# Kernel tuning notes

Measured on AMD Instinct MI355X. Metric: run time of the kernel, lower is better.

The kernel has to match this reference:

```python
import jax, jax.numpy as jnp
import numpy as np

N_NODES = 50000
N_EDGES = 400000
C = 32            # channels per irrep (scalars and l=1 vectors)
N_BASIS = 8
HID = 64          # radial MLP hidden dim
N_LAYERS = 2
N_SPECIES = 86
N_GRAPHS = 64
R_MAX = 5.0
EPS = 1e-5


def setup_inputs() -> dict:
    key = jax.random.key(0)
    ks = jax.random.split(key, 16)
    species = jax.random.randint(ks[0], (N_NODES,), 0, N_SPECIES)
    pos = jax.random.normal(ks[1], (N_NODES, 3), jnp.float32)
    edge_index = jax.random.randint(ks[2], (2, N_EDGES), 0, N_NODES)
    batch = jnp.sort(jax.random.randint(ks[3], (N_NODES,), 0, N_GRAPHS))

    emb = jax.random.normal(ks[4], (N_SPECIES, C), jnp.float32) * 0.1
    freqs = jnp.arange(1, N_BASIS + 1, dtype=jnp.float32) * jnp.pi / R_MAX  # trainable Bessel freqs
    rW1 = jax.random.normal(ks[5], (N_LAYERS, N_BASIS, HID), jnp.float32) / np.sqrt(N_BASIS)
    rb1 = jnp.zeros((N_LAYERS, HID), jnp.float32)
    rW2 = jax.random.normal(ks[6], (N_LAYERS, HID, HID), jnp.float32) / np.sqrt(HID)
    rb2 = jnp.zeros((N_LAYERS, HID), jnp.float32)
    rW3 = jax.random.normal(ks[7], (N_LAYERS, HID, 4 * C), jnp.float32) / np.sqrt(HID)
    rb3 = jnp.zeros((N_LAYERS, 4 * C), jnp.float32)
    Wss = jax.random.normal(ks[8], (N_LAYERS, C, C), jnp.float32) / np.sqrt(C)
    bss = jnp.zeros((N_LAYERS, C), jnp.float32)
    Wvv = jax.random.normal(ks[9], (N_LAYERS, C, C), jnp.float32) / np.sqrt(C)
    bn_gs = jnp.ones((N_LAYERS, C), jnp.float32)
    bn_bs = jnp.zeros((N_LAYERS, C), jnp.float32)
    bn_gv = jnp.ones((N_LAYERS, C), jnp.float32)
    W_out = jax.random.normal(ks[10], (C, 1), jnp.float32) / np.sqrt(C)
    b_out = jnp.zeros((1,), jnp.float32)
    atom_ref = jnp.zeros((N_SPECIES, 1), jnp.float32)  # AtomRef init zeros
    return dict(species=species, pos=pos, edge_index=edge_index, batch=batch,
                emb=emb, freqs=freqs, rW1=rW1, rb1=rb1, rW2=rW2, rb2=rb2,
                rW3=rW3, rb3=rb3, Wss=Wss, bss=bss, Wvv=Wvv,
                bn_gs=bn_gs, bn_bs=bn_bs, bn_gv=bn_gv,
                W_out=W_out, b_out=b_out, atom_ref=atom_ref)


def _bessel_basis(dist, freqs):
    # basis = sin(f*r)/r with smooth polynomial cutoff (as in BesselRadialBasis.forward)
    d = jnp.clip(dist, 0.0)
    basis = jnp.sin(freqs[None, :] * d[:, None]) / jnp.clip(d, 1e-6)[:, None]
    x = jnp.clip(d / R_MAX, 0.0, 1.0)
    cut = 1.0 - 6.0 * x ** 5 + 15.0 * x ** 4 - 10.0 * x ** 3
    cut = jnp.where(d <= R_MAX, cut, 0.0)
    return basis * cut[:, None]


def _forward(species, pos, edge_index, batch, emb, freqs, rW1, rb1, rW2, rb2,
             rW3, rb3, Wss, bss, Wvv, bn_gs, bn_bs, bn_gv, W_out, b_out, atom_ref):
    src, dst = edge_index[0], edge_index[1]
    vec = pos[dst] - pos[src]                      # (E,3) edge vectors
    dist = jnp.sqrt(jnp.sum(vec * vec, axis=-1))   # (E,)
    basis = _bessel_basis(dist, freqs)             # (E,NB)
    Y1 = vec / jnp.clip(dist, 1e-9)[:, None]       # (E,3) l=1 spherical harmonics (unit dir)

    s = emb[species]                               # (N,C) scalar features
    v = jnp.zeros((s.shape[0], C, 3), s.dtype)     # (N,C,3) l=1 features

    for l in range(N_LAYERS):
        # radial MLP -> per-edge channel-wise tensor-product weights (4 paths x C)
        h = jax.nn.silu(basis @ rW1[l] + rb1[l])
        h = jax.nn.silu(h @ rW2[l] + rb2[l])
        w = h @ rW3[l] + rb3[l]                    # (E,4C)
        w1, w2, w3, w4 = jnp.split(w, 4, axis=-1)  # each (E,C)

        xs = s[src]                                # (E,C)   gather
        xv = v[src]                                # (E,C,3) gather
        # TP paths: s*Y0 -> scalar; (v.Y1) -> gate scalar; s*Y1 -> vector; v*Y0 -> vector
        m_sf = w1 * xs                                               # (E,C)
        m_sg = w2 * jnp.einsum('ecd,ed->ec', xv, Y1)                 # (E,C)
        m_v = w3[..., None] * xs[..., None] * Y1[:, None, :] + w4[..., None] * xv  # (E,C,3)

        agg_sf = jax.ops.segment_sum(m_sf, dst, num_segments=N_NODES)
        agg_sg = jax.ops.segment_sum(m_sg, dst, num_segments=N_NODES)
        agg_v = jax.ops.segment_sum(m_v, dst, num_segments=N_NODES)

        # gated nonlinearity: silu on scalars, sigmoid gate on vectors
        s_new = jax.nn.silu(agg_sf)
        v_new = jax.nn.sigmoid(agg_sg)[..., None] * agg_v

        # self-interaction (equivariant linear mixing over channels)
        s_new = s_new @ Wss[l] + bss[l]
        v_new = jnp.einsum('ncd,cm->nmd', v_new, Wvv[l])

        # e3nn-style batch norm: standardize scalars; norm-normalize vectors
        mu = jnp.mean(s_new, axis=0)
        var = jnp.mean((s_new - mu) ** 2, axis=0)
        s_new = (s_new - mu) / jnp.sqrt(var + EPS) * bn_gs[l] + bn_bs[l]
        vnorm2 = jnp.mean(jnp.sum(v_new * v_new, axis=-1), axis=0) / 3.0  # per-channel, /(2l+1)
        v_new = v_new / jnp.sqrt(vnorm2 + EPS)[None, :, None] * bn_gv[l][None, :, None]

        # residual (irreps match)
        s = s + s_new
        v = v + v_new

    node_e = s @ W_out + b_out                                       # (N,1)
    graph_e = jax.ops.segment_sum(node_e, batch, num_segments=N_GRAPHS)
    ref_e = jax.ops.segment_sum(atom_ref[species], batch, num_segments=N_GRAPHS)
    return graph_e + ref_e                                           # (B,1)


def reference(species, pos, edge_index, batch, emb, freqs, rW1, rb1, rW2, rb2,
              rW3, rb3, Wss, bss, Wvv, bn_gs, bn_bs, bn_gv, W_out, b_out, atom_ref):
    return _forward(species, pos, edge_index, batch, emb, freqs, rW1, rb1, rW2, rb2,
                    rW3, rb3, Wss, bss, Wvv, bn_gs, bn_bs, bn_gv, W_out, b_out, atom_ref)
```

## Files before the change

### kernel.cpp

```cpp
#include <hip/hip_runtime.h>
#include <math.h>

#define N_NODES 50000
#define N_EDGES 400000
#define C 32
#define NB 8
#define HID 64
#define NL 2
#define NG 64
#define RMAXF 5.0f
#define EPSF 1e-5f
#define TBL 4096
#define BN_BLOCKS 512
#define NBLK_N ((N_NODES + 255) / 256)

__device__ __forceinline__ float silu_f(float x) { return x / (1.0f + __expf(-x)); }
__device__ __forceinline__ float sigmoid_f(float x) { return 1.0f / (1.0f + __expf(-x)); }
__device__ __forceinline__ void atomAddF(float* p, float val) {
  __hip_atomic_fetch_add(p, val, __ATOMIC_RELAXED, __HIP_MEMORY_SCOPE_AGENT);
}
__device__ __forceinline__ void atomAddD(double* p, double val) {
  __hip_atomic_fetch_add(p, val, __ATOMIC_RELAXED, __HIP_MEMORY_SCOPE_AGENT);
}
__device__ __forceinline__ unsigned short bf16_rne(float f) {
  unsigned u = __float_as_uint(f);
  return (unsigned short)((u + 0x7FFFu + ((u >> 16) & 1u)) >> 16);
}
__device__ __forceinline__ float bfu(unsigned short u) {
  return __uint_as_float(((unsigned)u) << 16);
}

__global__ __launch_bounds__(256) void k_edge_geom(
    const float* __restrict__ pos, const int* __restrict__ ei,
    const float* __restrict__ freqs,
    float* __restrict__ basis, float* __restrict__ Y1)
{
  int e = blockIdx.x * 256 + threadIdx.x;
  if (e >= N_EDGES) return;
  int s = ei[e], d = ei[N_EDGES + e];
  float vx = pos[d*3+0] - pos[s*3+0];
  float vy = pos[d*3+1] - pos[s*3+1];
  float vz = pos[d*3+2] - pos[s*3+2];
  float dist = sqrtf(vx*vx + vy*vy + vz*vz);
  float invd = 1.0f / fmaxf(dist, 1e-9f);
  Y1[e*3+0] = vx*invd; Y1[e*3+1] = vy*invd; Y1[e*3+2] = vz*invd;
  float x = fminf(fmaxf(dist * (1.0f/RMAXF), 0.0f), 1.0f);
  float x2 = x*x, x3 = x2*x;
  float cut = 1.0f - x3 * (10.0f - 15.0f*x + 6.0f*x2);
  if (dist > RMAXF) cut = 0.0f;
  float rinv = cut / fmaxf(dist, 1e-6f);
  #pragma unroll
  for (int k = 0; k < NB; k++)
    basis[e*NB + k] = sinf(freqs[k] * dist) * rinv;
}

__global__ __launch_bounds__(256) void k_node_init(
    const int* __restrict__ species, const float* __restrict__ emb,
    float* __restrict__ s, unsigned short* __restrict__ s_bf)
{
  int i = blockIdx.x * 256 + threadIdx.x;
  if (i >= N_NODES * C) return;
  int n = i >> 5, c = i & 31;
  float x = emb[species[n]*C + c];
  s[i] = x;
  s_bf[i] = bf16_rne(x);
}

__global__ __launch_bounds__(256) void k_hist(const int* __restrict__ ei, int* __restrict__ counts)
{
  int e = blockIdx.x * 256 + threadIdx.x;
  if (e >= N_EDGES) return;
  atomicAdd(&counts[ei[N_EDGES + e]], 1);
}

__global__ __launch_bounds__(256) void k_scanA(const int* __restrict__ counts, int* __restrict__ bsum)
{
  __shared__ int sh[256];
  int i = blockIdx.x * 256 + threadIdx.x;
  int x = (i < N_NODES) ? counts[i] : 0;
  sh[threadIdx.x] = x;
  __syncthreads();
  for (int off = 128; off > 0; off >>= 1) {
    if (threadIdx.x < off) sh[threadIdx.x] += sh[threadIdx.x + off];
    __syncthreads();
  }
  if (threadIdx.x == 0) bsum[blockIdx.x] = sh[0];
}

__global__ __launch_bounds__(256) void k_scanB(int* __restrict__ bsum)
{
  __shared__ int sh[256];
  int tid = threadIdx.x;
  int x = (tid < NBLK_N) ? bsum[tid] : 0;
  sh[tid] = x;
  __syncthreads();
  for (int off = 1; off < 256; off <<= 1) {
    int y = (tid >= off) ? sh[tid - off] : 0;
    __syncthreads();
    sh[tid] += y;
    __syncthreads();
  }
  if (tid < NBLK_N) bsum[tid] = sh[tid] - x;
}

__global__ __launch_bounds__(256) void k_scanC(const int* __restrict__ counts,
                                               const int* __restrict__ bsum,
                                               int* __restrict__ row_start)
{
  __shared__ int sh[256];
  int i = blockIdx.x * 256 + threadIdx.x;
  int x = (i < N_NODES) ? counts[i] : 0;
  sh[threadIdx.x] = x;
  __syncthreads();
  for (int off = 1; off < 256; off <<= 1) {
    int y = (threadIdx.x >= off) ? sh[threadIdx.x - off] : 0;
    __syncthreads();
    sh[threadIdx.x] += y;
    __syncthreads();
  }
  if (i < N_NODES) row_start[i] = bsum[blockIdx.x] + sh[threadIdx.x] - x;
}

__global__ __launch_bounds__(256) void k_geom_scatter(
    const float* __restrict__ pos, const int* __restrict__ ei,
    const int* __restrict__ row_start, int* __restrict__ cursor,
    float* __restrict__ rec)
{
  int e = blockIdx.x * 256 + threadIdx.x;
  if (e >= N_EDGES) return;
  int s = ei[e], d = ei[N_EDGES + e];
  float vx = pos[d*3+0] - pos[s*3+0];
  float vy = pos[d*3+1] - pos[s*3+1];
  float vz = pos[d*3+2] - pos[s*3+2];
  float dist = sqrtf(vx*vx + vy*vy + vz*vz);
  float invd = 1.0f / fmaxf(dist, 1e-9f);
  int p = row_start[d] + atomicAdd(&cursor[d], 1);
  float* rp = rec + (size_t)p * 8;
  float4 r0; r0.x = dist; r0.y = __int_as_float(s); r0.z = vx*invd; r0.w = vy*invd;
  *(float4*)rp = r0;
  rp[4] = vz*invd;
}

__global__ __launch_bounds__(256) void k_table_h(
    const float* __restrict__ freqs,
    const float* __restrict__ rW1, const float* __restrict__ rb1,
    const float* __restrict__ rW2, const float* __restrict__ rb2,
    float* __restrict__ h2tab)
{
  int idx = blockIdx.x * 256 + threadIdx.x;
  if (idx >= NL * TBL) return;
  int l = idx / TBL, i = idx - l * TBL;
  float d = (float)i * (RMAXF / (float)(TBL - 1));
  float x = fminf(fmaxf(d * (1.0f/RMAXF), 0.0f), 1.0f);
  float x2 = x*x, x3 = x2*x;
  float cut = 1.0f - x3 * (10.0f - 15.0f*x + 6.0f*x2);
  float rinv = cut / fmaxf(d, 1e-6f);
  float bas[NB];
  #pragma unroll
  for (int k = 0; k < NB; k++) bas[k] = sinf(freqs[k] * d) * rinv;

  const float* W1 = rW1 + l*NB*HID;
  const float* B1 = rb1 + l*HID;
  const float* W2 = rW2 + l*HID*HID;
  const float* B2 = rb2 + l*HID;

  float h2[HID];
  #pragma unroll
  for (int j = 0; j < HID; j++) h2[j] = B2[j];
  #pragma unroll 2
  for (int k = 0; k < HID; k++) {
    float t = B1[k];
    #pragma unroll
    for (int b = 0; b < NB; b++) t = fmaf(bas[b], W1[b*HID + k], t);
    float h1k = silu_f(t);
    const float* r = W2 + k*HID;
    #pragma unroll
    for (int j = 0; j < HID; j++) h2[j] = fmaf(h1k, r[j], h2[j]);
  }
  float* out = h2tab + (size_t)idx * HID;
  #pragma unroll
  for (int j = 0; j < HID; j++) out[j] = silu_f(h2[j]);
}

__global__ __launch_bounds__(256) void k_table_w(
    const float* __restrict__ h2tab,
    const float* __restrict__ rW3, const float* __restrict__ rb3,
    float* __restrict__ wtab)
{
  int idx = blockIdx.x * 256 + threadIdx.x;
  if (idx >= NL * TBL * 16) return;
  int chunk = idx & 15;
  int row   = idx >> 4;
  int l     = row / TBL;
  const float* h2 = h2tab + (size_t)row * HID;
  const float* W3 = rW3 + l*HID*4*C + chunk*8;
  const float* B3 = rb3 + l*4*C + chunk*8;
  float a[8];
  #pragma unroll
  for (int ci = 0; ci < 8; ci++) a[ci] = B3[ci];
  #pragma unroll 4
  for (int k = 0; k < HID; k++) {
    float h = h2[k];
    #pragma unroll
    for (int ci = 0; ci < 8; ci++) a[ci] = fmaf(h, W3[k*4*C + ci], a[ci]);
  }
  float* out = wtab + (size_t)row * 128 + chunk*8;
  #pragma unroll
  for (int ci = 0; ci < 8; ci++) out[ci] = a[ci];
}

__global__ __launch_bounds__(256) void k_agg_update(
    const float* __restrict__ tb,
    const float* __restrict__ rec,
    const int* __restrict__ row_start, const int* __restrict__ counts,
    const unsigned short* __restrict__ s_bf, const unsigned short* __restrict__ v_bf,
    const float* __restrict__ Wss, const float* __restrict__ bss,
    const float* __restrict__ Wvv,
    float* __restrict__ s_new, float* __restrict__ v_new)
{
  int t = blockIdx.x * 256 + threadIdx.x;
  int n = t >> 5;
  int c = t & 31;

  const float SCALE = (float)(TBL - 1) / RMAXF;
  float asf = 0.0f, asg = 0.0f, av0 = 0.0f, av1 = 0.0f, av2 = 0.0f;
  int beg = row_start[n], cnt = counts[n];

  if (cnt > 0) {
    int last = beg + cnt - 1;
    int pA = beg, pB = (beg + 1 < last) ? beg + 1 : last;
    float4 rA = *(const float4*)(rec + (size_t)pA * 8);
    float  zA = rec[(size_t)pA * 8 + 4];
    float4 rB = *(const float4*)(rec + (size_t)pB * 8);
    float  zB = rec[(size_t)pB * 8 + 4];

    for (int i = 0; i < cnt; i += 2) {
      int pA2 = beg + i + 2; pA2 = pA2 < last ? pA2 : last;
      int pB2 = beg + i + 3; pB2 = pB2 < last ? pB2 : last;
      float4 rA_n = *(const float4*)(rec + (size_t)pA2 * 8);
      float  zA_n = rec[(size_t)pA2 * 8 + 4];
      float4 rB_n = *(const float4*)(rec + (size_t)pB2 * 8);
      float  zB_n = rec[(size_t)pB2 * 8 + 4];

      float validB = (i + 1 < cnt) ? 1.0f : 0.0f;
      float dA = rA.x;  int srcA = __float_as_int(rA.y);
      float yA0 = rA.z, yA1 = rA.w, yA2 = zA;
      float dB = rB.x;  int srcB = __float_as_int(rB.y);
      float yB0 = rB.z, yB1 = rB.w, yB2 = zB;

      float xsA = bfu(s_bf[srcA*C + c]);
      const unsigned short* vpA = v_bf + (size_t)(srcA*C + c)*3;
      float xvA0 = bfu(vpA[0]), xvA1 = bfu(vpA[1]), xvA2 = bfu(vpA[2]);
      float xsB = bfu(s_bf[srcB*C + c]);
      const unsigned short* vpB = v_bf + (size_t)(srcB*C + c)*3;
      float xvB0 = bfu(vpB[0]), xvB1 = bfu(vpB[1]), xvB2 = bfu(vpB[2]);

      float tsA = fminf(dA, RMAXF) * SCALE;
      int t0A = (int)tsA; t0A = t0A > TBL-2 ? TBL-2 : t0A;
      float frA = tsA - (float)t0A;
      float tsB = fminf(dB, RMAXF) * SCALE;
      int t0B = (int)tsB; t0B = t0B > TBL-2 ? TBL-2 : t0B;
      float frB = tsB - (float)t0B;

      const float* rtA0 = tb + (size_t)t0A * 128 + c;
      const float* rtA1 = rtA0 + 128;
      const float* rtB0 = tb + (size_t)t0B * 128 + c;
      const float* rtB1 = rtB0 + 128;

      float w1A = fmaf(frA, rtA1[0]  - rtA0[0],  rtA0[0]);
      float w2A = fmaf(frA, rtA1[32] - rtA0[32], rtA0[32]);
      float w3A = fmaf(frA, rtA1[64] - rtA0[64], rtA0[64]);
      float w4A = fmaf(frA, rtA1[96] - rtA0[96], rtA0[96]);
      float w1B = validB * fmaf(frB, rtB1[0]  - rtB0[0],  rtB0[0]);
      float w2B = validB * fmaf(frB, rtB1[32] - rtB0[32], rtB0[32]);
      float w3B = validB * fmaf(frB, rtB1[64] - rtB0[64], rtB0[64]);
      float w4B = validB * fmaf(frB, rtB1[96] - rtB0[96], rtB0[96]);

      asf = fmaf(w1A, xsA, asf);
      asg = fmaf(w2A, xvA0*yA0 + xvA1*yA1 + xvA2*yA2, asg);
      float w3xsA = w3A * xsA;
      av0 += fmaf(w3xsA, yA0, w4A*xvA0);
      av1 += fmaf(w3xsA, yA1, w4A*xvA1);
      av2 += fmaf(w3xsA, yA2, w4A*xvA2);

      asf = fmaf(w1B, xsB, asf);
      asg = fmaf(w2B, xvB0*yB0 + xvB1*yB1 + xvB2*yB2, asg);
      float w3xsB = w3B * xsB;
      av0 += fmaf(w3xsB, yB0, w4B*xvB0);
      av1 += fmaf(w3xsB, yB1, w4B*xvB1);
      av2 += fmaf(w3xsB, yB2, w4B*xvB2);

      rA = rA_n; zA = zA_n; rB = rB_n; zB = zB_n;
    }
  }

  float sgv  = silu_f(asf);
  float gate = sigmoid_f(asg);
  float vg0 = gate*av0, vg1 = gate*av1, vg2 = gate*av2;

  float sn = bss[c];
  float vm0 = 0.0f, vm1 = 0.0f, vm2 = 0.0f;
  #pragma unroll
  for (int k = 0; k < C; k++) {
    float a  = __shfl(sgv, k, 32);
    sn = fmaf(a, Wss[k*C + c], sn);
    float wv = Wvv[k*C + c];
    vm0 = fmaf(__shfl(vg0, k, 32), wv, vm0);
    vm1 = fmaf(__shfl(vg1, k, 32), wv, vm1);
    vm2 = fmaf(__shfl(vg2, k, 32), wv, vm2);
  }

  s_new[n*C + c] = sn;
  float* vo = v_new + (size_t)(n*C + c)*3;
  vo[0] = vm0; vo[1] = vm1; vo[2] = vm2;
}

__global__ __launch_bounds__(256) void k_bn_stats(
    const float* __restrict__ s_new, const float* __restrict__ v_new,
    double* __restrict__ bn_sums)
{
  __shared__ float lacc[3*C];
  if (threadIdx.x < 3*C) lacc[threadIdx.x] = 0.0f;
  __syncthreads();
  int c = threadIdx.x & 31;
  float r1 = 0.0f, r2 = 0.0f, r3 = 0.0f;
  const int NC = N_NODES * C;
  for (int i = blockIdx.x * 256 + threadIdx.x; i < NC; i += BN_BLOCKS * 256) {
    float sn = s_new[i];
    const float* vp = v_new + (size_t)i * 3;
    r1 += sn;
    r2 += sn * sn;
    r3 += vp[0]*vp[0] + vp[1]*vp[1] + vp[2]*vp[2];
  }
  atomicAdd(&lacc[c],       r1);
  atomicAdd(&lacc[C + c],   r2);
  atomicAdd(&lacc[2*C + c], r3);
  __syncthreads();
  if (threadIdx.x < 3*C) atomAddD(&bn_sums[threadIdx.x], (double)lacc[threadIdx.x]);
}

__global__ __launch_bounds__(256) void k_apply(
    const float* __restrict__ s_new, const float* __restrict__ v_new,
    const double* __restrict__ bn_sums,
    const float* __restrict__ gs, const float* __restrict__ gv,
    const float* __restrict__ bn_bs,
    float* __restrict__ s, float* __restrict__ v,
    unsigned short* __restrict__ s_bf, unsigned short* __restrict__ v_bf)
{
  int i = blockIdx.x * 256 + threadIdx.x;
  if (i >= N_NODES * C) return;
  int c = i & 31;
  double S1 = bn_sums[c], S2 = bn_sums[C + c], VN = bn_sums[2*C + c];
  float mu  = (float)(S1 / (double)N_NODES);
  float var = (float)(S2 / (double)N_NODES) - mu*mu;
  float vn2 = (float)(VN / (3.0 * (double)N_NODES));
  float ssc = gs[c] / sqrtf(var + EPSF);
  float vsc = gv[c] / sqrtf(vn2 + EPSF);

  float sv = s[i] + (s_new[i] - mu) * ssc + bn_bs[c];
  s[i] = sv;
  s_bf[i] = bf16_rne(sv);
  float* vp = v + (size_t)i*3;
  const float* vn = v_new + (size_t)i*3;
  unsigned short* vb = v_bf + (size_t)i*3;
  #pragma unroll
  for (int d = 0; d < 3; d++) {
    float vv = vp[d] + vn[d] * vsc;
    vp[d] = vv;
    vb[d] = bf16_rne(vv);
  }
}

__global__ __launch_bounds__(256) void k_readout(
    const float* __restrict__ s, const int* __restrict__ species,
    const int* __restrict__ batch,
    const float* __restrict__ W_out, const float* __restrict__ b_out,
    const float* __restrict__ atom_ref, float* __restrict__ out)
{
  __shared__ float acc[NG];
  if (threadIdx.x < NG) acc[threadIdx.x] = 0.0f;
  __syncthreads();
  int n = blockIdx.x * 256 + threadIdx.x;
  if (n < N_NODES) {
    float e = b_out[0] + atom_ref[species[n]];
    #pragma unroll
    for (int c = 0; c < C; c++) e = fmaf(s[n*C + c], W_out[c], e);
    atomicAdd(&acc[batch[n]], e);
  }
  __syncthreads();
  if (threadIdx.x < NG) {
    float a = acc[threadIdx.x];
    if (a != 0.0f) atomAddF(&out[threadIdx.x], a);
  }
}

__global__ __launch_bounds__(256) void k_edge_msg_fb(
    const float* __restrict__ basis, const float* __restrict__ Y1,
    const int* __restrict__ ei,
    const float* __restrict__ s, const float* __restrict__ v,
    const float* __restrict__ rW1, const float* __restrict__ rb1,
    const float* __restrict__ rW2, const float* __restrict__ rb2,
    const float* __restrict__ rW3, const float* __restrict__ rb3,
    float* __restrict__ agg_sf, float* __restrict__ agg_sg, float* __restrict__ agg_v)
{
  int e = blockIdx.x * 256 + threadIdx.x;
  if (e >= N_EDGES) return;
  int src = ei[e], dst = ei[N_EDGES + e];
  const float4 b0 = *(const float4*)(basis + (size_t)e*NB);
  const float4 b1 = *(const float4*)(basis + (size_t)e*NB + 4);
  float bas[NB] = {b0.x, b0.y, b0.z, b0.w, b1.x, b1.y, b1.z, b1.w};
  float h2[HID];
  #pragma unroll
  for (int j = 0; j < HID; j++) h2[j] = rb2[j];
  #pragma unroll 2
  for (int k = 0; k < HID; k++) {
    float t = rb1[k];
    #pragma unroll
    for (int b = 0; b < NB; b++) t = fmaf(bas[b], rW1[b*HID + k], t);
    float h1k = silu_f(t);
    const float* r = rW2 + k*HID;
    #pragma unroll
    for (int j = 0; j < HID; j++) h2[j] = fmaf(h1k, r[j], h2[j]);
  }
  #pragma unroll
  for (int j = 0; j < HID; j++) h2[j] = silu_f(h2[j]);
  float y0 = Y1[e*3+0], y1 = Y1[e*3+1], y2 = Y1[e*3+2];
  #pragma unroll 1
  for (int cb = 0; cb < 16; cb++) {
    float a[8];
    #pragma unroll
    for (int ci = 0; ci < 8; ci++) a[ci] = rb3[cb*8 + ci];
    #pragma unroll
    for (int k = 0; k < HID; k++) {
      float h = h2[k];
      #pragma unroll
      for (int ci = 0; ci < 8; ci++) a[ci] = fmaf(h, rW3[k*4*C + cb*8 + ci], a[ci]);
    }
    #pragma unroll
    for (int ci = 0; ci < 8; ci++) {
      int o = cb*8 + ci;
      int path = o >> 5;
      int c = o & 31;
      float xs = s[src*C + c];
      const float* vp = v + (size_t)(src*C + c)*3;
      float xv0 = vp[0], xv1 = vp[1], xv2 = vp[2];
      if (path == 0) {
        atomAddF(&agg_sf[dst*C + c], a[ci] * xs);
      } else if (path == 1) {
        atomAddF(&agg_sg[dst*C + c], a[ci] * (xv0*y0 + xv1*y1 + xv2*y2));
      } else if (path == 2) {
        float w3xs = a[ci] * xs;
        float* ap = agg_v + (size_t)(dst*C + c)*3;
        atomAddF(ap+0, w3xs*y0); atomAddF(ap+1, w3xs*y1); atomAddF(ap+2, w3xs*y2);
      } else {
        float* ap = agg_v + (size_t)(dst*C + c)*3;
        atomAddF(ap+0, a[ci]*xv0); atomAddF(ap+1, a[ci]*xv1); atomAddF(ap+2, a[ci]*xv2);
      }
    }
  }
}

__global__ __launch_bounds__(256) void k_node_update_fb(
    const float* __restrict__ agg_sf, const float* __restrict__ agg_sg,
    const float* __restrict__ agg_v,
    const float* __restrict__ Wss, const float* __restrict__ bss,
    const float* __restrict__ Wvv,
    float* __restrict__ s_new, float* __restrict__ v_new,
    double* __restrict__ bn_sums)
{
  __shared__ float lacc[3*C];
  int t = blockIdx.x * 256 + threadIdx.x;
  int n = t >> 5;
  int c = t & 31;
  if (threadIdx.x < 3*C) lacc[threadIdx.x] = 0.0f;
  __syncthreads();
  float asf = agg_sf[n*C + c];
  float asg = agg_sg[n*C + c];
  const float* ap = agg_v + (size_t)(n*C + c)*3;
  float av0 = ap[0], av1 = ap[1], av2 = ap[2];
  float sgv = silu_f(asf);
  float gate = sigmoid_f(asg);
  float vg0 = gate*av0, vg1 = gate*av1, vg2 = gate*av2;
  float sn = bss[c];
  float vm0 = 0.0f, vm1 = 0.0f, vm2 = 0.0f;
  #pragma unroll
  for (int k = 0; k < C; k++) {
    float a  = __shfl(sgv, k, 32);
    sn = fmaf(a, Wss[k*C + c], sn);
    float wv = Wvv[k*C + c];
    vm0 = fmaf(__shfl(vg0, k, 32), wv, vm0);
    vm1 = fmaf(__shfl(vg1, k, 32), wv, vm1);
    vm2 = fmaf(__shfl(vg2, k, 32), wv, vm2);
  }
  s_new[n*C + c] = sn;
  float* vo = v_new + (size_t)(n*C + c)*3;
  vo[0] = vm0; vo[1] = vm1; vo[2] = vm2;
  float vn2 = vm0*vm0 + vm1*vm1 + vm2*vm2;
  atomicAdd(&lacc[c], sn);
  atomicAdd(&lacc[C + c], sn*sn);
  atomicAdd(&lacc[2*C + c], vn2);
  __syncthreads();
  if (threadIdx.x < 3*C) atomAddD(&bn_sums[threadIdx.x], (double)lacc[threadIdx.x]);
}

__global__ void k_bn_scales_fb(const double* __restrict__ bn_sums,
                               const float* __restrict__ gs, const float* __restrict__ gv,
                               float* __restrict__ scales)
{
  int m = threadIdx.x;
  if (m >= C) return;
  double S1 = bn_sums[m], S2 = bn_sums[C + m], VN = bn_sums[2*C + m];
  double mu  = S1 / (double)N_NODES;
  double var = S2 / (double)N_NODES - mu*mu;
  double vn2 = VN / (3.0 * (double)N_NODES);
  scales[m]       = (float)mu;
  scales[C + m]   = gs[m] / sqrtf((float)var + EPSF);
  scales[2*C + m] = gv[m] / sqrtf((float)vn2 + EPSF);
}

__global__ __launch_bounds__(256) void k_apply_fb(
    const float* __restrict__ s_new, const float* __restrict__ v_new,
    const float* __restrict__ scales, const float* __restrict__ bn_bs,
    float* __restrict__ s, float* __restrict__ v)
{
  int i = blockIdx.x * 256 + threadIdx.x;
  if (i >= N_NODES * C) return;
  int c = i & 31;
  s[i] += (s_new[i] - scales[c]) * scales[C + c] + bn_bs[c];
  float vs = scales[2*C + c];
  v[(size_t)i*3+0] += v_new[(size_t)i*3+0] * vs;
  v[(size_t)i*3+1] += v_new[(size_t)i*3+1] * vs;
  v[(size_t)i*3+2] += v_new[(size_t)i*3+2] * vs;
}

extern "C" void kernel_launch(void* const* d_in, const int* in_sizes, int n_in,
                              void* d_out, int out_size, void* d_ws, size_t ws_size,
                              hipStream_t stream)
{
  const int*   species  = (const int*)  d_in[0];
  const float* pos      = (const float*)d_in[1];
  const int*   ei       = (const int*)  d_in[2];
  const int*   batch    = (const int*)  d_in[3];
  const float* emb      = (const float*)d_in[4];
  const float* freqs    = (const float*)d_in[5];
  const float* rW1      = (const float*)d_in[6];
  const float* rb1      = (const float*)d_in[7];
  const float* rW2      = (const float*)d_in[8];
  const float* rb2      = (const float*)d_in[9];
  const float* rW3      = (const float*)d_in[10];
  const float* rb3      = (const float*)d_in[11];
  const float* Wss      = (const float*)d_in[12];
  const float* bss      = (const float*)d_in[13];
  const float* Wvv      = (const float*)d_in[14];
  const float* bn_gs    = (const float*)d_in[15];
  const float* bn_bs    = (const float*)d_in[16];
  const float* bn_gv    = (const float*)d_in[17];
  const float* W_out    = (const float*)d_in[18];
  const float* b_out    = (const float*)d_in[19];
  const float* atom_ref = (const float*)d_in[20];

  float* ws = (float*)d_ws;
  size_t off = 0;
  float* basis  = ws + off; off += (size_t)N_EDGES * NB;
  float* Y1     = ws + off; off += (size_t)N_EDGES * 3;
  float* s      = ws + off; off += (size_t)N_NODES * C;
  float* v      = ws + off; off += (size_t)N_NODES * C * 3;
  float* s_new  = ws + off; off += (size_t)N_NODES * C;
  float* v_new  = ws + off; off += (size_t)N_NODES * C * 3;
  double* bn_sums = (double*)(ws + off); off += 192;
  float* scales = ws + off; off += 96;

  size_t ra = off;
  float* rec      = ws + ra;            ra += (size_t)N_EDGES * 8;
  int*   counts   = (int*)(ws + ra);    ra += N_NODES;
  int*   row_start= (int*)(ws + ra);    ra += N_NODES;
  int*   cursor   = (int*)(ws + ra);    ra += N_NODES;
  int*   bsum     = (int*)(ws + ra);    ra += 256;
  float* h2tab    = ws + ra;            ra += (size_t)NL * TBL * HID;
  float* wtab     = ws + ra;            ra += (size_t)NL * TBL * 128;
  unsigned short* s_bf = (unsigned short*)(ws + ra); ra += (size_t)N_NODES * C / 2;
  unsigned short* v_bf = (unsigned short*)(ws + ra); ra += (size_t)N_NODES * C * 3 / 2;
  size_t req_sorted = ra * 4;

  size_t rb = off;
  float* agg_sf = ws + rb; rb += (size_t)N_NODES * C;
  float* agg_sg = ws + rb; rb += (size_t)N_NODES * C;
  float* agg_v  = ws + rb; rb += (size_t)N_NODES * C * 3;

  dim3 b256(256);
  const int gE  = (N_EDGES + 255) / 256;
  const int gNC = (N_NODES * C + 255) / 256;
  const int gN  = (N_NODES + 255) / 256;

  hipMemsetAsync(v, 0, (size_t)N_NODES * C * 3 * sizeof(float), stream);

  if (ws_size >= req_sorted) {
    hipMemsetAsync(v_bf, 0, (size_t)N_NODES * C * 3 * sizeof(unsigned short), stream);
    hipMemsetAsync(counts, 0, N_NODES * sizeof(int), stream);
    hipMemsetAsync(cursor, 0, N_NODES * sizeof(int), stream);
    k_node_init<<<gNC, b256, 0, stream>>>(species, emb, s, s_bf);
    k_hist<<<gE, b256, 0, stream>>>(ei, counts);
    k_scanA<<<NBLK_N, b256, 0, stream>>>(counts, bsum);
    k_scanB<<<1, b256, 0, stream>>>(bsum);
    k_scanC<<<NBLK_N, b256, 0, stream>>>(counts, bsum, row_start);
    k_geom_scatter<<<gE, b256, 0, stream>>>(pos, ei, row_start, cursor, rec);
    k_table_h<<<(NL*TBL)/256, b256, 0, stream>>>(freqs, rW1, rb1, rW2, rb2, h2tab);
    k_table_w<<<(NL*TBL*16)/256, b256, 0, stream>>>(h2tab, rW3, rb3, wtab);

    for (int l = 0; l < NL; l++) {
      hipMemsetAsync(bn_sums, 0, 96 * sizeof(double), stream);
      k_agg_update<<<(N_NODES*C)/256, b256, 0, stream>>>(
          wtab + (size_t)l * TBL * 128, rec,
          row_start, counts, s_bf, v_bf, Wss + l*C*C, bss + l*C, Wvv + l*C*C,
          s_new, v_new);
      k_bn_stats<<<BN_BLOCKS, b256, 0, stream>>>(s_new, v_new, bn_sums);
      k_apply<<<gNC, b256, 0, stream>>>(s_new, v_new, bn_sums,
          bn_gs + l*C, bn_gv + l*C, bn_bs + l*C, s, v, s_bf, v_bf);
    }
  } else {
    k_node_init<<<gNC, b256, 0, stream>>>(species, emb, s, (unsigned short*)(ws + off));
    k_edge_geom<<<gE, b256, 0, stream>>>(pos, ei, freqs, basis, Y1);
    for (int l = 0; l < NL; l++) {
      hipMemsetAsync(agg_sf, 0, (size_t)N_NODES * 5 * C * sizeof(float), stream);
      hipMemsetAsync(bn_sums, 0, 96 * sizeof(double), stream);
      k_edge_msg_fb<<<gE, b256, 0, stream>>>(basis, Y1, ei, s, v,
          rW1 + l*NB*HID, rb1 + l*HID, rW2 + l*HID*HID, rb2 + l*HID,
          rW3 + l*HID*4*C, rb3 + l*4*C, agg_sf, agg_sg, agg_v);
      k_node_update_fb<<<(N_NODES*C)/256, b256, 0, stream>>>(agg_sf, agg_sg, agg_v,
          Wss + l*C*C, bss + l*C, Wvv + l*C*C, s_new, v_new, bn_sums);
      k_bn_scales_fb<<<1, 64, 0, stream>>>(bn_sums, bn_gs + l*C, bn_gv + l*C, scales);
      k_apply_fb<<<gNC, b256, 0, stream>>>(s_new, v_new, scales, bn_bs + l*C, s, v);
    }
  }

  hipMemsetAsync(d_out, 0, NG * sizeof(float), stream);
  k_readout<<<gN, b256, 0, stream>>>(s, species, batch, W_out, b_out, atom_ref, (float*)d_out);
}
```

Before: 321.2 us.

## Specialize first layer for zero vectors, pad bf16 vectors, fuse readout into apply

The aggregation kernel is templated on whether vector features exist. Layer 0 therefore skips the vector gathers and the w2/w4 table loads, since v starts at zero. Vector bf16 storage is padded to 4 halves so each gather is a single ushort4 load, and the first apply writes v directly instead of needing a memset. The readout is fused into the last apply kernel through a wave shuffle reduction plus one atomic per node, which removes a separate kernel and several memsets at the cost of more atomics and 33% more vector bf16 memory.

```diff
diff --git a/kernel.cpp b/kernel.cpp
--- a/kernel.cpp
+++ b/kernel.cpp
@@ -209,11 +209,12 @@
   for (int ci = 0; ci < 8; ci++) out[ci] = a[ci];
 }
 
+template<bool HAS_V>
 __global__ __launch_bounds__(256) void k_agg_update(
     const float* __restrict__ tb,
     const float* __restrict__ rec,
     const int* __restrict__ row_start, const int* __restrict__ counts,
-    const unsigned short* __restrict__ s_bf, const unsigned short* __restrict__ v_bf,
+    const unsigned short* __restrict__ s_bf, const unsigned short* __restrict__ v_bf4,
     const float* __restrict__ Wss, const float* __restrict__ bss,
     const float* __restrict__ Wvv,
     float* __restrict__ s_new, float* __restrict__ v_new)
@@ -249,11 +250,15 @@
       float yB0 = rB.z, yB1 = rB.w, yB2 = zB;
 
       float xsA = bfu(s_bf[srcA*C + c]);
-      const unsigned short* vpA = v_bf + (size_t)(srcA*C + c)*3;
-      float xvA0 = bfu(vpA[0]), xvA1 = bfu(vpA[1]), xvA2 = bfu(vpA[2]);
       float xsB = bfu(s_bf[srcB*C + c]);
-      const unsigned short* vpB = v_bf + (size_t)(srcB*C + c)*3;
-      float xvB0 = bfu(vpB[0]), xvB1 = bfu(vpB[1]), xvB2 = bfu(vpB[2]);
+      float xvA0 = 0.0f, xvA1 = 0.0f, xvA2 = 0.0f;
+      float xvB0 = 0.0f, xvB1 = 0.0f, xvB2 = 0.0f;
+      if (HAS_V) {
+        ushort4 a4 = *(const ushort4*)(v_bf4 + (size_t)(srcA*C + c)*4);
+        ushort4 b4 = *(const ushort4*)(v_bf4 + (size_t)(srcB*C + c)*4);
+        xvA0 = bfu(a4.x); xvA1 = bfu(a4.y); xvA2 = bfu(a4.z);
+        xvB0 = bfu(b4.x); xvB1 = bfu(b4.y); xvB2 = bfu(b4.z);
+      }
 
       float tsA = fminf(dA, RMAXF) * SCALE;
       int t0A = (int)tsA; t0A = t0A > TBL-2 ? TBL-2 : t0A;
@@ -268,27 +273,30 @@
       const float* rtB1 = rtB0 + 128;
 
       float w1A = fmaf(frA, rtA1[0]  - rtA0[0],  rtA0[0]);
-      float w2A = fmaf(frA, rtA1[32] - rtA0[32], rtA0[32]);
       float w3A = fmaf(frA, rtA1[64] - rtA0[64], rtA0[64]);
-      float w4A = fmaf(frA, rtA1[96] - rtA0[96], rtA0[96]);
       float w1B = validB * fmaf(frB, rtB1[0]  - rtB0[0],  rtB0[0]);
-      float w2B = validB * fmaf(frB, rtB1[32] - rtB0[32], rtB0[32]);
       float w3B = validB * fmaf(frB, rtB1[64] - rtB0[64], rtB0[64]);
-      float w4B = validB * fmaf(frB, rtB1[96] - rtB0[96], rtB0[96]);
 
       asf = fmaf(w1A, xsA, asf);
-      asg = fmaf(w2A, xvA0*yA0 + xvA1*yA1 + xvA2*yA2, asg);
       float w3xsA = w3A * xsA;
-      av0 += fmaf(w3xsA, yA0, w4A*xvA0);
-      av1 += fmaf(w3xsA, yA1, w4A*xvA1);
-      av2 += fmaf(w3xsA, yA2, w4A*xvA2);
-
       asf = fmaf(w1B, xsB, asf);
-      asg = fmaf(w2B, xvB0*yB0 + xvB1*yB1 + xvB2*yB2, asg);
       float w3xsB = w3B * xsB;
-      av0 += fmaf(w3xsB, yB0, w4B*xvB0);
-      av1 += fmaf(w3xsB, yB1, w4B*xvB1);
-      av2 += fmaf(w3xsB, yB2, w4B*xvB2);
+
+      if (HAS_V) {
+        float w2A = fmaf(frA, rtA1[32] - rtA0[32], rtA0[32]);
+        float w4A = fmaf(frA, rtA1[96] - rtA0[96], rtA0[96]);
+        float w2B = validB * fmaf(frB, rtB1[32] - rtB0[32], rtB0[32]);
+        float w4B = validB * fmaf(frB, rtB1[96] - rtB0[96], rtB0[96]);
+        asg = fmaf(w2A, xvA0*yA0 + xvA1*yA1 + xvA2*yA2, asg);
+        asg = fmaf(w2B, xvB0*yB0 + xvB1*yB1 + xvB2*yB2, asg);
+        av0 += fmaf(w3xsA, yA0, w4A*xvA0) + fmaf(w3xsB, yB0, w4B*xvB0);
+        av1 += fmaf(w3xsA, yA1, w4A*xvA1) + fmaf(w3xsB, yB1, w4B*xvB1);
+        av2 += fmaf(w3xsA, yA2, w4A*xvA2) + fmaf(w3xsB, yB2, w4B*xvB2);
+      } else {
+        av0 += fmaf(w3xsA, yA0, w3xsB * yB0);
+        av1 += fmaf(w3xsA, yA1, w3xsB * yB1);
+        av2 += fmaf(w3xsA, yA2, w3xsB * yB2);
+      }
 
       rA = rA_n; zA = zA_n; rB = rB_n; zB = zB_n;
     }
@@ -339,17 +347,22 @@
   if (threadIdx.x < 3*C) atomAddD(&bn_sums[threadIdx.x], (double)lacc[threadIdx.x]);
 }
 
+template<bool FIRST, bool LAST>
 __global__ __launch_bounds__(256) void k_apply(
     const float* __restrict__ s_new, const float* __restrict__ v_new,
     const double* __restrict__ bn_sums,
     const float* __restrict__ gs, const float* __restrict__ gv,
     const float* __restrict__ bn_bs,
     float* __restrict__ s, float* __restrict__ v,
-    unsigned short* __restrict__ s_bf, unsigned short* __restrict__ v_bf)
+    unsigned short* __restrict__ s_bf, unsigned short* __restrict__ v_bf4,
+    const int* __restrict__ species, const int* __restrict__ batch,
+    const float* __restrict__ W_out, const float* __restrict__ b_out,
+    const float* __restrict__ atom_ref, float* __restrict__ out)
 {
   int i = blockIdx.x * 256 + threadIdx.x;
   if (i >= N_NODES * C) return;
   int c = i & 31;
+  int n = i >> 5;
   double S1 = bn_sums[c], S2 = bn_sums[C + c], VN = bn_sums[2*C + c];
   float mu  = (float)(S1 / (double)N_NODES);
   float var = (float)(S2 / (double)N_NODES) - mu*mu;
@@ -362,35 +375,22 @@
   s_bf[i] = bf16_rne(sv);
   float* vp = v + (size_t)i*3;
   const float* vn = v_new + (size_t)i*3;
-  unsigned short* vb = v_bf + (size_t)i*3;
-  #pragma unroll
-  for (int d = 0; d < 3; d++) {
-    float vv = vp[d] + vn[d] * vsc;
-    vp[d] = vv;
-    vb[d] = bf16_rne(vv);
-  }
-}
-
-__global__ __launch_bounds__(256) void k_readout(
-    const float* __restrict__ s, const int* __restrict__ species,
-    const int* __restrict__ batch,
-    const float* __restrict__ W_out, const float* __restrict__ b_out,
-    const float* __restrict__ atom_ref, float* __restrict__ out)
-{
-  __shared__ float acc[NG];
-  if (threadIdx.x < NG) acc[threadIdx.x] = 0.0f;
-  __syncthreads();
-  int n = blockIdx.x * 256 + threadIdx.x;
-  if (n < N_NODES) {
-    float e = b_out[0] + atom_ref[species[n]];
-    #pragma unroll
-    for (int c = 0; c < C; c++) e = fmaf(s[n*C + c], W_out[c], e);
-    atomicAdd(&acc[batch[n]], e);
-  }
-  __syncthreads();
-  if (threadIdx.x < NG) {
-    float a = acc[threadIdx.x];
-    if (a != 0.0f) atomAddF(&out[threadIdx.x], a);
+  ushort4 vb;
+  float vv0 = (FIRST ? 0.0f : vp[0]) + vn[0] * vsc;
+  float vv1 = (FIRST ? 0.0f : vp[1]) + vn[1] * vsc;
+  float vv2 = (FIRST ? 0.0f : vp[2]) + vn[2] * vsc;
+  vp[0] = vv0; vp[1] = vv1; vp[2] = vv2;
+  vb.x = bf16_rne(vv0); vb.y = bf16_rne(vv1); vb.z = bf16_rne(vv2); vb.w = 0;
+  *(ushort4*)(v_bf4 + (size_t)i*4) = vb;
+
+  if (LAST) {
+    float e = sv * W_out[c];
+    #pragma unroll
+    for (int off = 16; off > 0; off >>= 1) e += __shfl_down(e, off, 32);
+    if (c == 0) {
+      e += b_out[0] + atom_ref[species[n]];
+      atomAddF(&out[batch[n]], e);
+    }
   }
 }
 
@@ -531,6 +531,29 @@
   v[(size_t)i*3+0] += v_new[(size_t)i*3+0] * vs;
   v[(size_t)i*3+1] += v_new[(size_t)i*3+1] * vs;
   v[(size_t)i*3+2] += v_new[(size_t)i*3+2] * vs;
+}
+
+__global__ __launch_bounds__(256) void k_readout_fb(
+    const float* __restrict__ s, const int* __restrict__ species,
+    const int* __restrict__ batch,
+    const float* __restrict__ W_out, const float* __restrict__ b_out,
+    const float* __restrict__ atom_ref, float* __restrict__ out)
+{
+  __shared__ float acc[NG];
+  if (threadIdx.x < NG) acc[threadIdx.x] = 0.0f;
+  __syncthreads();
+  int n = blockIdx.x * 256 + threadIdx.x;
+  if (n < N_NODES) {
+    float e = b_out[0] + atom_ref[species[n]];
+    #pragma unroll
+    for (int c = 0; c < C; c++) e = fmaf(s[n*C + c], W_out[c], e);
+    atomicAdd(&acc[batch[n]], e);
+  }
+  __syncthreads();
+  if (threadIdx.x < NG) {
+    float a = acc[threadIdx.x];
+    if (a != 0.0f) atomAddF(&out[threadIdx.x], a);
+  }
 }
 
 extern "C" void kernel_launch(void* const* d_in, const int* in_sizes, int n_in,
@@ -578,8 +601,8 @@
   int*   bsum     = (int*)(ws + ra);    ra += 256;
   float* h2tab    = ws + ra;            ra += (size_t)NL * TBL * HID;
   float* wtab     = ws + ra;            ra += (size_t)NL * TBL * 128;
-  unsigned short* s_bf = (unsigned short*)(ws + ra); ra += (size_t)N_NODES * C / 2;
-  unsigned short* v_bf = (unsigned short*)(ws + ra); ra += (size_t)N_NODES * C * 3 / 2;
+  unsigned short* s_bf  = (unsigned short*)(ws + ra); ra += (size_t)N_NODES * C / 2;
+  unsigned short* v_bf4 = (unsigned short*)(ws + ra); ra += (size_t)N_NODES * C * 2;
   size_t req_sorted = ra * 4;
 
   size_t rb = off;
@@ -592,12 +615,10 @@
   const int gNC = (N_NODES * C + 255) / 256;
   const int gN  = (N_NODES + 255) / 256;
 
-  hipMemsetAsync(v, 0, (size_t)N_NODES * C * 3 * sizeof(float), stream);
-
   if (ws_size >= req_sorted) {
-    hipMemsetAsync(v_bf, 0, (size_t)N_NODES * C * 3 * sizeof(unsigned short), stream);
     hipMemsetAsync(counts, 0, N_NODES * sizeof(int), stream);
     hipMemsetAsync(cursor, 0, N_NODES * sizeof(int), stream);
+    hipMemsetAsync(d_out, 0, NG * sizeof(float), stream);
     k_node_init<<<gNC, b256, 0, stream>>>(species, emb, s, s_bf);
     k_hist<<<gE, b256, 0, stream>>>(ei, counts);
     k_scanA<<<NBLK_N, b256, 0, stream>>>(counts, bsum);
@@ -607,17 +628,25 @@
     k_table_h<<<(NL*TBL)/256, b256, 0, stream>>>(freqs, rW1, rb1, rW2, rb2, h2tab);
     k_table_w<<<(NL*TBL*16)/256, b256, 0, stream>>>(h2tab, rW3, rb3, wtab);
 
-    for (int l = 0; l < NL; l++) {
-      hipMemsetAsync(bn_sums, 0, 96 * sizeof(double), stream);
-      k_agg_update<<<(N_NODES*C)/256, b256, 0, stream>>>(
-          wtab + (size_t)l * TBL * 128, rec,
-          row_start, counts, s_bf, v_bf, Wss + l*C*C, bss + l*C, Wvv + l*C*C,
-          s_new, v_new);
-      k_bn_stats<<<BN_BLOCKS, b256, 0, stream>>>(s_new, v_new, bn_sums);
-      k_apply<<<gNC, b256, 0, stream>>>(s_new, v_new, bn_sums,
-          bn_gs + l*C, bn_gv + l*C, bn_bs + l*C, s, v, s_bf, v_bf);
-    }
+    hipMemsetAsync(bn_sums, 0, 96 * sizeof(double), stream);
+    k_agg_update<false><<<(N_NODES*C)/256, b256, 0, stream>>>(
+        wtab, rec, row_start, counts, s_bf, v_bf4,
+        Wss, bss, Wvv, s_new, v_new);
+    k_bn_stats<<<BN_BLOCKS, b256, 0, stream>>>(s_new, v_new, bn_sums);
+    k_apply<true, false><<<gNC, b256, 0, stream>>>(s_new, v_new, bn_sums,
+        bn_gs, bn_gv, bn_bs, s, v, s_bf, v_bf4,
+        species, batch, W_out, b_out, atom_ref, (float*)d_out);
+
+    hipMemsetAsync(bn_sums, 0, 96 * sizeof(double), stream);
+    k_agg_update<true><<<(N_NODES*C)/256, b256, 0, stream>>>(
+        wtab + (size_t)TBL * 128, rec, row_start, counts, s_bf, v_bf4,
+        Wss + C*C, bss + C, Wvv + C*C, s_new, v_new);
+    k_bn_stats<<<BN_BLOCKS, b256, 0, stream>>>(s_new, v_new, bn_sums);
+    k_apply<false, true><<<gNC, b256, 0, stream>>>(s_new, v_new, bn_sums,
+        bn_gs + C, bn_gv + C, bn_bs + C, s, v, s_bf, v_bf4,
+        species, batch, W_out, b_out, atom_ref, (float*)d_out);
   } else {
+    hipMemsetAsync(v, 0, (size_t)N_NODES * C * 3 * sizeof(float), stream);
     k_node_init<<<gNC, b256, 0, stream>>>(species, emb, s, (unsigned short*)(ws + off));
     k_edge_geom<<<gE, b256, 0, stream>>>(pos, ei, freqs, basis, Y1);
     for (int l = 0; l < NL; l++) {
@@ -631,8 +660,7 @@
       k_bn_scales_fb<<<1, 64, 0, stream>>>(bn_sums, bn_gs + l*C, bn_gv + l*C, scales);
       k_apply_fb<<<gNC, b256, 0, stream>>>(s_new, v_new, scales, bn_bs + l*C, s, v);
     }
-  }
-
-  hipMemsetAsync(d_out, 0, NG * sizeof(float), stream);
-  k_readout<<<gN, b256, 0, stream>>>(s, species, batch, W_out, b_out, atom_ref, (float*)d_out);
-}
+    hipMemsetAsync(d_out, 0, NG * sizeof(float), stream);
+    k_readout_fb<<<gN, b256, 0, stream>>>(s, species, batch, W_out, b_out, atom_ref, (float*)d_out);
+  }
+}
```

New measurement: 669.8 us. 109% more time.
